# Optimization experiments

Measured on AMD Instinct MI355X. Metric: run time of the kernel, lower is better.

Reference implementation:

```python
import jax, jax.numpy as jnp
import numpy as np

# init kwargs baked as constants: crop_height -> depth dim, crop_length -> H, crop_width -> W
CROP_D, CROP_H, CROP_W = 16, 16, 16
EXTRAP = 0.0


def setup_inputs() -> dict:
    key = jax.random.key(0)
    k1, k2, k3 = jax.random.split(key, 3)
    N, C, D, H, W = 8, 32, 64, 64, 64
    NB = 256
    image = jax.random.normal(k1, (N, C, D, H, W), dtype=jnp.float32)
    # boxes: normalized (x1, y1, z1, x2, y2, z2) with lo <= hi per axis
    raw = jax.random.uniform(k2, (NB, 3, 2), dtype=jnp.float32)
    lo = jnp.min(raw, axis=2)
    hi = jnp.max(raw, axis=2)
    boxes = jnp.concatenate([lo, hi], axis=1)  # [NB, 6]
    box_ind = jax.random.randint(k3, (NB,), 0, N, dtype=jnp.int32)
    return {"image": image, "boxes": boxes, "box_ind": box_ind}


def _coords(lo, hi, L, c):
    # lo, hi: [nb] normalized box edges; returns [nb, c] continuous source coords
    if c > 1:
        i = jnp.arange(c, dtype=lo.dtype)
        step = (hi - lo) * (L - 1) / (c - 1)          # [nb]
        return lo[:, None] * (L - 1) + i[None, :] * step[:, None]
    return (0.5 * (lo + hi) * (L - 1))[:, None]


def _lerp_idx(coord, L):
    valid = (coord >= 0) & (coord <= L - 1)
    c = jnp.clip(coord, 0, L - 1)
    i0 = jnp.floor(c).astype(jnp.int32)
    i1 = jnp.minimum(i0 + 1, L - 1)
    frac = c - i0.astype(coord.dtype)
    return i0, i1, frac, valid


def reference(image, boxes, box_ind):
    N, C, D, H, W = image.shape
    x1, y1, z1, x2, y2, z2 = [boxes[:, k] for k in range(6)]
    zc = _coords(z1, z2, D, CROP_D)  # [nb, cd]
    yc = _coords(y1, y2, H, CROP_H)  # [nb, ch]
    xc = _coords(x1, x2, W, CROP_W)  # [nb, cw]
    z0, z1i, fz, vz = _lerp_idx(zc, D)
    y0, y1i, fy, vy = _lerp_idx(yc, H)
    x0, x1i, fx, vx = _lerp_idx(xc, W)

    img = jnp.moveaxis(image, 1, -1)  # [N, D, H, W, C] -> channels-last gather
    b = box_ind[:, None, None, None]

    def g(zi, yi, xi):
        # [nb, cd, ch, cw, C]
        return img[b, zi[:, :, None, None], yi[:, None, :, None], xi[:, None, None, :], :]

    fz_ = fz[:, :, None, None, None]
    fy_ = fy[:, None, :, None, None]
    fx_ = fx[:, None, None, :, None]

    c00 = g(z0, y0, x0) * (1 - fx_) + g(z0, y0, x1i) * fx_
    c01 = g(z0, y1i, x0) * (1 - fx_) + g(z0, y1i, x1i) * fx_
    c10 = g(z1i, y0, x0) * (1 - fx_) + g(z1i, y0, x1i) * fx_
    c11 = g(z1i, y1i, x0) * (1 - fx_) + g(z1i, y1i, x1i) * fx_
    c0 = c00 * (1 - fy_) + c01 * fy_
    c1 = c10 * (1 - fy_) + c11 * fy_
    out = c0 * (1 - fz_) + c1 * fz_  # [nb, cd, ch, cw, C]

    valid = (vz[:, :, None, None] & vy[:, None, :, None] & vx[:, None, None, :])[..., None]
    out = jnp.where(valid, out, jnp.asarray(EXTRAP, out.dtype))
    return jnp.moveaxis(out, -1, 1)  # [nb, C, cd, ch, cw]
```

## Files before the change

kernel.cpp:

```cpp
#include <hip/hip_runtime.h>
#include <stdint.h>

#define NBOX 256
#define NC   32
#define ND   64
#define NH   64
#define NW   64
#define CD   16
#define CH   16
#define CW   16
#define NXCD 8
#define DHW  (ND * NH * NW)

__global__ __launch_bounds__(NBOX) void CropAndResize3D_perm_kernel(
    const int* __restrict__ box_ind, int* __restrict__ perm)
{
    __shared__ int nsh[NBOX];
    const int t = threadIdx.x;
    nsh[t] = box_ind[t];
    __syncthreads();
    const int n_t = nsh[t];
    int rank = 0;
    #pragma unroll 8
    for (int j = 0; j < NBOX; ++j) {
        const int n_j = nsh[j];
        rank += (n_j < n_t) || (n_j == n_t && j < t);
    }
    perm[rank] = t;
}

__global__ __launch_bounds__(256) void CropAndResize3D_89481348645400_kernel(
    const float* __restrict__ image,
    const float* __restrict__ boxes,
    const int*   __restrict__ box_ind,
    const int*   __restrict__ perm,
    float*       __restrict__ out)
{
    __shared__ float sh[2 * 64 * 64];

    const int nwg_per_xcd = (NBOX * CD) / NXCD;
    const int hwid = blockIdx.x;
    const int blk = (hwid & (NXCD - 1)) * nwg_per_xcd + (hwid >> 3);

    const int slot = blk >> 4;
    const int b = perm ? perm[slot] : slot;
    const int z = blk & 15;
    const int t  = threadIdx.x;
    const int w  = t >> 6;
    const int l  = t & 63;
    const int q  = l >> 4;
    const int tx = l & 15;
    const int ty = (w << 2) | q;

    const float bx1 = boxes[b*6+0], by1 = boxes[b*6+1], bz1 = boxes[b*6+2];
    const float bx2 = boxes[b*6+3], by2 = boxes[b*6+4], bz2 = boxes[b*6+5];
    const int   n   = box_ind[b];

    const float zstep = (bz2 - bz1) * 63.0f / 15.0f;
    const float ystep = (by2 - by1) * 63.0f / 15.0f;
    const float xstep = (bx2 - bx1) * 63.0f / 15.0f;

    const float zc = bz1 * 63.0f + (float)z * zstep;
    const bool  vz = (zc >= 0.0f) && (zc <= 63.0f);
    const float zq = fminf(fmaxf(zc, 0.0f), 63.0f);
    const int   z0 = (int)floorf(zq);
    const int   z1 = min(z0 + 1, ND - 1);
    const float fz = zq - (float)z0;

    const float yc = by1 * 63.0f + (float)ty * ystep;
    const bool  vy = (yc >= 0.0f) && (yc <= 63.0f);
    const float yq = fminf(fmaxf(yc, 0.0f), 63.0f);
    const float fy = yq - floorf(yq);

    const float xcf = bx1 * 63.0f + (float)tx * xstep;
    const bool  vx  = (xcf >= 0.0f) && (xcf <= 63.0f);
    const float xq  = fminf(fmaxf(xcf, 0.0f), 63.0f);
    const int   x0  = (int)floorf(xq);
    const int   x1  = min(x0 + 1, NW - 1);
    const float fx  = xq - (float)x0;

    const bool valid = vz && vy && vx;
    const float gz = 1.0f - fz, gy = 1.0f - fy, gx = 1.0f - fx;

    const float xcl = bx1 * 63.0f;
    const float xch = bx1 * 63.0f + 15.0f * xstep;
    const int x0min = (int)floorf(fminf(fmaxf(xcl, 0.0f), 63.0f));
    const int x1max = min((int)floorf(fminf(fmaxf(xch, 0.0f), 63.0f)) + 1, NW - 1);
    const int xlo4  = x0min & ~3;
    const int G     = ((x1max - xlo4) >> 2) + 1;

    int soff0, soff1, soff2, soff3;
    {
        int tmp[4];
        #pragma unroll
        for (int k = 0; k < 4; ++k) {
            const int rho = k * 4 + q;
            const int zc_ = rho >> 3;
            const int qq  = (rho >> 1) & 3;
            const int yc_ = rho & 1;
            const int zs  = zc_ ? z1 : z0;
            const int yo  = (w << 2) | qq;
            const float yco = by1 * 63.0f + (float)yo * ystep;
            const float yqs = fminf(fmaxf(yco, 0.0f), 63.0f);
            const int   ys0 = (int)floorf(yqs);
            const int   ysel = yc_ ? min(ys0 + 1, NH - 1) : ys0;
            const int   key = rho & 7;
            const int   g   = tx ^ key;
            const int   sx  = (g < G) ? (xlo4 + (g << 2)) : xlo4;
            tmp[k] = (zs * NH + ysel) * NW + sx;
        }
        soff0 = tmp[0]; soff1 = tmp[1]; soff2 = tmp[2]; soff3 = tmp[3];
    }
    const int wbF = w << 10;

    const int dx0 = x0 - xlo4;
    const int dx1 = x1 - xlo4;
    #define SWZ(rho, dx) ((((((dx) >> 2) ^ ((rho) & 7))) << 2) | ((dx) & 3))
    const int a000 = wbF + (2*q    ) * 64 + SWZ(2*q    , dx0);
    const int a001 = wbF + (2*q    ) * 64 + SWZ(2*q    , dx1);
    const int a010 = wbF + (2*q + 1) * 64 + SWZ(2*q + 1, dx0);
    const int a011 = wbF + (2*q + 1) * 64 + SWZ(2*q + 1, dx1);
    #undef SWZ

    const float* imgb = image + (size_t)n * (NC * DHW);
    float* op = out + (size_t)b * (NC * CD * CH * CW) + (z * CH + ty) * CW + tx;

    #define ISSUE(c)  do {                                                     \
        const float* p_ = imgb + (size_t)(c) * DHW;                            \
        float* l_ = sh + (((c) & 1) << 12) + wbF;                              \
        __builtin_amdgcn_global_load_lds(                                      \
            (const __attribute__((address_space(1))) uint32_t*)(p_ + soff0),   \
            (__attribute__((address_space(3))) uint32_t*)(l_      ), 16, 0, 0);\
        __builtin_amdgcn_global_load_lds(                                      \
            (const __attribute__((address_space(1))) uint32_t*)(p_ + soff1),   \
            (__attribute__((address_space(3))) uint32_t*)(l_ + 256), 16, 0, 0);\
        __builtin_amdgcn_global_load_lds(                                      \
            (const __attribute__((address_space(1))) uint32_t*)(p_ + soff2),   \
            (__attribute__((address_space(3))) uint32_t*)(l_ + 512), 16, 0, 0);\
        __builtin_amdgcn_global_load_lds(                                      \
            (const __attribute__((address_space(1))) uint32_t*)(p_ + soff3),   \
            (__attribute__((address_space(3))) uint32_t*)(l_ + 768), 16, 0, 0);\
    } while (0)

    #define COMPUTE(c)  do {                                                   \
        const float* S_ = sh + (((c) & 1) << 12);                              \
        const float s000 = S_[a000], s100 = S_[a000 + 512];                    \
        const float s001 = S_[a001], s101 = S_[a001 + 512];                    \
        const float s010 = S_[a010], s110 = S_[a010 + 512];                    \
        const float s011 = S_[a011], s111 = S_[a011 + 512];                    \
        const float c00 = s000 * gx + s001 * fx;                               \
        const float c01 = s010 * gx + s011 * fx;                               \
        const float c10 = s100 * gx + s101 * fx;                               \
        const float c11 = s110 * gx + s111 * fx;                               \
        const float c0  = c00 * gy + c01 * fy;                                 \
        const float c1  = c10 * gy + c11 * fy;                                 \
        float v = c0 * gz + c1 * fz;                                           \
        v = valid ? v : 0.0f;                                                  \
        __builtin_nontemporal_store(v, op + (c) * (CD * CH * CW));             \
    } while (0)

    ISSUE(0);
    ISSUE(1);

    #pragma unroll
    for (int c = 0; c < NC; ++c) {
        if (c == 0)      asm volatile("s_waitcnt vmcnt(4)" ::: "memory");
        else if (c < 31) asm volatile("s_waitcnt vmcnt(5)" ::: "memory");
        else             asm volatile("s_waitcnt vmcnt(1)" ::: "memory");
        __builtin_amdgcn_sched_barrier(0);
        COMPUTE(c);
        asm volatile("s_waitcnt lgkmcnt(0)" ::: "memory");
        __builtin_amdgcn_sched_barrier(0);
        if (c + 2 < NC) ISSUE(c + 2);
    }

    #undef ISSUE
    #undef COMPUTE
}

extern "C" void kernel_launch(void* const* d_in, const int* in_sizes, int n_in,
                              void* d_out, int out_size, void* d_ws, size_t ws_size,
                              hipStream_t stream) {
    const float* image   = (const float*)d_in[0];
    const float* boxes   = (const float*)d_in[1];
    const int*   box_ind = (const int*)d_in[2];
    float*       out     = (float*)d_out;

    int* perm = nullptr;
    if (ws_size >= NBOX * sizeof(int)) {
        perm = (int*)d_ws;
        CropAndResize3D_perm_kernel<<<1, NBOX, 0, stream>>>(box_ind, perm);
    }

    const int blocks = NBOX * CD;
    CropAndResize3D_89481348645400_kernel<<<blocks, 256, 0, stream>>>(
        image, boxes, box_ind, perm, out);
}
```

Before: 120.2 us.

## Interpolate z/y in registers and stage only x-pass partials in LDS

Each thread now loads its own four 16-float row segments (z0/z1 × y0/y1) into registers with plain float4 loads, replacing the global-to-LDS direct loads. It blends them with precomputed z·y weights and writes one swizzled partial row to a double-buffered LDS tile. The x interpolation then needs only two LDS reads per output. This shrinks shared memory from 32 KB to 8 KB and cuts LDS reads per output from eight to two, in exchange for more VGPRs, hand-placed raw s_barrier synchronisation between the write and read phases, and the loss of the async LDS-load path.

Result: slower. 129.2 us (+7.4%).

```diff
diff --git a/kernel.cpp b/kernel.cpp
--- a/kernel.cpp
+++ b/kernel.cpp
@@ -36,7 +36,7 @@
     const int*   __restrict__ perm,
     float*       __restrict__ out)
 {
-    __shared__ float sh[2 * 64 * 64];
+    __shared__ float sh[2 * 16 * 64];
 
     const int nwg_per_xcd = (NBOX * CD) / NXCD;
     const int hwid = blockIdx.x;
@@ -46,11 +46,8 @@
     const int b = perm ? perm[slot] : slot;
     const int z = blk & 15;
     const int t  = threadIdx.x;
-    const int w  = t >> 6;
-    const int l  = t & 63;
-    const int q  = l >> 4;
-    const int tx = l & 15;
-    const int ty = (w << 2) | q;
+    const int ty = t >> 4;
+    const int tx = t & 15;
 
     const float bx1 = boxes[b*6+0], by1 = boxes[b*6+1], bz1 = boxes[b*6+2];
     const float bx2 = boxes[b*6+3], by2 = boxes[b*6+4], bz2 = boxes[b*6+5];
@@ -70,7 +67,9 @@
     const float yc = by1 * 63.0f + (float)ty * ystep;
     const bool  vy = (yc >= 0.0f) && (yc <= 63.0f);
     const float yq = fminf(fmaxf(yc, 0.0f), 63.0f);
-    const float fy = yq - floorf(yq);
+    const int   y0 = (int)floorf(yq);
+    const int   y1 = min(y0 + 1, NH - 1);
+    const float fy = yq - (float)y0;
 
     const float xcf = bx1 * 63.0f + (float)tx * xstep;
     const bool  vx  = (xcf >= 0.0f) && (xcf <= 63.0f);
@@ -82,99 +81,76 @@
     const bool valid = vz && vy && vx;
     const float gz = 1.0f - fz, gy = 1.0f - fy, gx = 1.0f - fx;
 
+    const float w00 = gz * gy, w01 = gz * fy, w10 = fz * gy, w11 = fz * fy;
+
     const float xcl = bx1 * 63.0f;
     const float xch = bx1 * 63.0f + 15.0f * xstep;
     const int x0min = (int)floorf(fminf(fmaxf(xcl, 0.0f), 63.0f));
-    const int x1max = min((int)floorf(fminf(fmaxf(xch, 0.0f), 63.0f)) + 1, NW - 1);
     const int xlo4  = x0min & ~3;
-    const int G     = ((x1max - xlo4) >> 2) + 1;
 
-    int soff0, soff1, soff2, soff3;
-    {
-        int tmp[4];
-        #pragma unroll
-        for (int k = 0; k < 4; ++k) {
-            const int rho = k * 4 + q;
-            const int zc_ = rho >> 3;
-            const int qq  = (rho >> 1) & 3;
-            const int yc_ = rho & 1;
-            const int zs  = zc_ ? z1 : z0;
-            const int yo  = (w << 2) | qq;
-            const float yco = by1 * 63.0f + (float)yo * ystep;
-            const float yqs = fminf(fmaxf(yco, 0.0f), 63.0f);
-            const int   ys0 = (int)floorf(yqs);
-            const int   ysel = yc_ ? min(ys0 + 1, NH - 1) : ys0;
-            const int   key = rho & 7;
-            const int   g   = tx ^ key;
-            const int   sx  = (g < G) ? (xlo4 + (g << 2)) : xlo4;
-            tmp[k] = (zs * NH + ysel) * NW + sx;
-        }
-        soff0 = tmp[0]; soff1 = tmp[1]; soff2 = tmp[2]; soff3 = tmp[3];
-    }
-    const int wbF = w << 10;
+    const int sx = min(xlo4 + (tx << 2), NW - 4);
+    const int soff0 = (z0 * NH + y0) * NW + sx;
+    const int soff1 = (z0 * NH + y1) * NW + sx;
+    const int soff2 = (z1 * NH + y0) * NW + sx;
+    const int soff3 = (z1 * NH + y1) * NW + sx;
 
-    const int dx0 = x0 - xlo4;
-    const int dx1 = x1 - xlo4;
-    #define SWZ(rho, dx) ((((((dx) >> 2) ^ ((rho) & 7))) << 2) | ((dx) & 3))
-    const int a000 = wbF + (2*q    ) * 64 + SWZ(2*q    , dx0);
-    const int a001 = wbF + (2*q    ) * 64 + SWZ(2*q    , dx1);
-    const int a010 = wbF + (2*q + 1) * 64 + SWZ(2*q + 1, dx0);
-    const int a011 = wbF + (2*q + 1) * 64 + SWZ(2*q + 1, dx1);
-    #undef SWZ
+    const int key  = (ty & 3) << 1;
+    const int wadr = ty * 64 + ((tx ^ key) << 2);
+    const int dx0  = x0 - xlo4;
+    const int dx1  = x1 - xlo4;
+    const int a0   = ty * 64 + ((((dx0 >> 2) ^ key)) << 2) + (dx0 & 3);
+    const int a1   = ty * 64 + ((((dx1 >> 2) ^ key)) << 2) + (dx1 & 3);
 
     const float* imgb = image + (size_t)n * (NC * DHW);
     float* op = out + (size_t)b * (NC * CD * CH * CW) + (z * CH + ty) * CW + tx;
 
-    #define ISSUE(c)  do {                                                     \
+    float4 A0, A1, A2, A3, B0, B1, B2, B3;
+
+    #define ISSUE(Ra, Rb, Rc, Rd, c)  do {                                     \
         const float* p_ = imgb + (size_t)(c) * DHW;                            \
-        float* l_ = sh + (((c) & 1) << 12) + wbF;                              \
-        __builtin_amdgcn_global_load_lds(                                      \
-            (const __attribute__((address_space(1))) uint32_t*)(p_ + soff0),   \
-            (__attribute__((address_space(3))) uint32_t*)(l_      ), 16, 0, 0);\
-        __builtin_amdgcn_global_load_lds(                                      \
-            (const __attribute__((address_space(1))) uint32_t*)(p_ + soff1),   \
-            (__attribute__((address_space(3))) uint32_t*)(l_ + 256), 16, 0, 0);\
-        __builtin_amdgcn_global_load_lds(                                      \
-            (const __attribute__((address_space(1))) uint32_t*)(p_ + soff2),   \
-            (__attribute__((address_space(3))) uint32_t*)(l_ + 512), 16, 0, 0);\
-        __builtin_amdgcn_global_load_lds(                                      \
-            (const __attribute__((address_space(1))) uint32_t*)(p_ + soff3),   \
-            (__attribute__((address_space(3))) uint32_t*)(l_ + 768), 16, 0, 0);\
+        Ra = *(const float4*)(p_ + soff0);                                     \
+        Rb = *(const float4*)(p_ + soff1);                                     \
+        Rc = *(const float4*)(p_ + soff2);                                     \
+        Rd = *(const float4*)(p_ + soff3);                                     \
+    } while (0)
+
+    #define CWRITE(Ra, Rb, Rc, Rd, c)  do {                                    \
+        float4 o_;                                                             \
+        o_.x = Ra.x * w00 + Rb.x * w01 + Rc.x * w10 + Rd.x * w11;              \
+        o_.y = Ra.y * w00 + Rb.y * w01 + Rc.y * w10 + Rd.y * w11;              \
+        o_.z = Ra.z * w00 + Rb.z * w01 + Rc.z * w10 + Rd.z * w11;              \
+        o_.w = Ra.w * w00 + Rb.w * w01 + Rc.w * w10 + Rd.w * w11;              \
+        *(float4*)(sh + (((c) & 1) << 10) + wadr) = o_;                        \
     } while (0)
 
     #define COMPUTE(c)  do {                                                   \
-        const float* S_ = sh + (((c) & 1) << 12);                              \
-        const float s000 = S_[a000], s100 = S_[a000 + 512];                    \
-        const float s001 = S_[a001], s101 = S_[a001 + 512];                    \
-        const float s010 = S_[a010], s110 = S_[a010 + 512];                    \
-        const float s011 = S_[a011], s111 = S_[a011 + 512];                    \
-        const float c00 = s000 * gx + s001 * fx;                               \
-        const float c01 = s010 * gx + s011 * fx;                               \
-        const float c10 = s100 * gx + s101 * fx;                               \
-        const float c11 = s110 * gx + s111 * fx;                               \
-        const float c0  = c00 * gy + c01 * fy;                                 \
-        const float c1  = c10 * gy + c11 * fy;                                 \
-        float v = c0 * gz + c1 * fz;                                           \
+        const float* S_ = sh + (((c) & 1) << 10);                              \
+        const float s0 = S_[a0], s1 = S_[a1];                                  \
+        float v = s0 * gx + s1 * fx;                                           \
         v = valid ? v : 0.0f;                                                  \
         __builtin_nontemporal_store(v, op + (c) * (CD * CH * CW));             \
     } while (0)
 
-    ISSUE(0);
-    ISSUE(1);
+    ISSUE(A0, A1, A2, A3, 0);
+    CWRITE(A0, A1, A2, A3, 0);
+    ISSUE(B0, B1, B2, B3, 1);
 
     #pragma unroll
-    for (int c = 0; c < NC; ++c) {
-        if (c == 0)      asm volatile("s_waitcnt vmcnt(4)" ::: "memory");
-        else if (c < 31) asm volatile("s_waitcnt vmcnt(5)" ::: "memory");
-        else             asm volatile("s_waitcnt vmcnt(1)" ::: "memory");
-        __builtin_amdgcn_sched_barrier(0);
+    for (int c = 0; c < NC; c += 2) {
+        if (c + 2 < NC) ISSUE(A0, A1, A2, A3, c + 2);
         COMPUTE(c);
-        asm volatile("s_waitcnt lgkmcnt(0)" ::: "memory");
-        __builtin_amdgcn_sched_barrier(0);
-        if (c + 2 < NC) ISSUE(c + 2);
+        if (c + 1 < NC) CWRITE(B0, B1, B2, B3, c + 1);
+        __builtin_amdgcn_s_barrier();
+        if (c + 1 < NC) {
+            if (c + 3 < NC) ISSUE(B0, B1, B2, B3, c + 3);
+            COMPUTE(c + 1);
+            if (c + 2 < NC) CWRITE(A0, A1, A2, A3, c + 2);
+            __builtin_amdgcn_s_barrier();
+        }
     }
 
     #undef ISSUE
+    #undef CWRITE
     #undef COMPUTE
 }
 
```
